# Optimization experiments

Measured on AMD Instinct MI355X. Metric: run time of the kernel, lower is better.

The kernel has to match this reference:

```python
import jax, jax.numpy as jnp
from jax import lax
import numpy as np

H = 64
NS = 20000
NR = 2000
T = 24
ALPHA = 0.5


def _p(key, *shape):
    return jax.random.normal(key, shape, dtype=jnp.float32) * 0.05


def setup_inputs() -> dict:
    key = jax.random.key(0)
    ks = jax.random.split(key, 40)
    inp = {
        "x_store": jax.random.normal(ks[0], (NS, T), dtype=jnp.float32),
        "x_region": jax.random.normal(ks[1], (NR, T), dtype=jnp.float32),
        "edge_ss": jax.random.randint(ks[2], (2, 640000), 0, NS),
        "edge_rs_src": jax.random.randint(ks[3], (160000,), 0, NR),
        "edge_rs_dst": jax.random.randint(ks[4], (160000,), 0, NS),
        "edge_sr_src": jax.random.randint(ks[5], (160000,), 0, NS),
        "edge_sr_dst": jax.random.randint(ks[6], (160000,), 0, NR),
        # LSTM pretransform params (torch gate order i,f,g,o)
        "Wih_s": _p(ks[7], 4 * H, 1), "Whh_s": _p(ks[8], 4 * H, H),
        "bih_s": _p(ks[9], 4 * H), "bhh_s": _p(ks[10], 4 * H),
        "Wih_r": _p(ks[11], 4 * H, 1), "Whh_r": _p(ks[12], 4 * H, H),
        "bih_r": _p(ks[13], 4 * H), "bhh_r": _p(ks[14], 4 * H),
        # DirSageConv (store-store)
        "W_s2d": _p(ks[15], H, H), "b_s2d": _p(ks[16], H),
        "W_d2s": _p(ks[17], H, H), "b_d2s": _p(ks[18], H),
        "W_self": _p(ks[19], H, H), "b_self": _p(ks[20], H),
        # SAGEConv region->store (lin_l w/ bias, lin_r no bias)
        "Wl_rs": _p(ks[21], H, H), "bl_rs": _p(ks[22], H), "Wr_rs": _p(ks[23], H, H),
        # SAGEConv store->region
        "Wl_sr": _p(ks[24], H, H), "bl_sr": _p(ks[25], H), "Wr_sr": _p(ks[26], H, H),
        # final linear
        "Wf": _p(ks[27], H, H), "bf": _p(ks[28], H),
    }
    return inp


def lstm_last(x, Wih, Whh, bih, bhh):
    # x: [N, T] scalar sequences (input_size=1). Returns last hidden state [N, H].
    N = x.shape[0]
    w_in = Wih[:, 0]  # [4H]
    b = bih + bhh

    def step(carry, xt):
        h, c = carry
        gates = xt[:, None] * w_in[None, :] + h @ Whh.T + b  # [N, 4H]
        i, f, g, o = jnp.split(gates, 4, axis=1)
        c = jax.nn.sigmoid(f) * c + jax.nn.sigmoid(i) * jnp.tanh(g)
        h = jax.nn.sigmoid(o) * jnp.tanh(c)
        return (h, c), None

    z = jnp.zeros((N, Whh.shape[1]), x.dtype)
    (h, _), _ = lax.scan(step, (z, z), x.T)
    return h


def mean_aggr(feats, dst_idx, num_dst):
    # mean of gathered edge messages per destination node (0 for isolated nodes)
    s = jax.ops.segment_sum(feats, dst_idx, num_segments=num_dst)
    cnt = jax.ops.segment_sum(jnp.ones(dst_idx.shape, feats.dtype), dst_idx, num_segments=num_dst)
    return s / jnp.maximum(cnt, 1.0)[:, None]


def reference(x_store, x_region, edge_ss, edge_rs_src, edge_rs_dst,
              edge_sr_src, edge_sr_dst,
              Wih_s, Whh_s, bih_s, bhh_s, Wih_r, Whh_r, bih_r, bhh_r,
              W_s2d, b_s2d, W_d2s, b_d2s, W_self, b_self,
              Wl_rs, bl_rs, Wr_rs, Wl_sr, bl_sr, Wr_sr, Wf, bf):
    # per-node-type LSTM pretransform -> [N, H]
    hs = lstm_last(x_store, Wih_s, Whh_s, bih_s, bhh_s)
    hr = lstm_last(x_region, Wih_r, Whh_r, bih_r, bhh_r)

    # DirSageConv on (store, link, store)
    src, dst = edge_ss[0], edge_ss[1]
    a_fwd = mean_aggr(hs[src], dst, NS) @ W_s2d.T + b_s2d   # src -> dst
    a_rev = mean_aggr(hs[dst], src, NS) @ W_d2s.T + b_d2s   # dst -> src
    dir_out = hs @ W_self.T + b_self + (1.0 - ALPHA) * a_fwd + ALPHA * a_rev

    # SAGEConv (region, influences, store)
    rs_out = mean_aggr(hr[edge_rs_src], edge_rs_dst, NS) @ Wl_rs.T + bl_rs + hs @ Wr_rs.T

    # SAGEConv (store, rev_influences, region)
    sr_out = mean_aggr(hs[edge_sr_src], edge_sr_dst, NR) @ Wl_sr.T + bl_sr + hr @ Wr_sr.T

    # HeteroConv aggr='mean' over edge types per dst node type
    store_h = (dir_out + rs_out) * 0.5
    region_h = sr_out

    # residual + relu
    store_h = jax.nn.relu(store_h + hs)
    region_h = jax.nn.relu(region_h + hr)  # computed as in torch, unused by output

    return store_h @ Wf.T + bf
```

## Files before the change

kernel.cpp:

```cpp
#include <hip/hip_runtime.h>
#include <hip/hip_bf16.h>

#define TT 24
#define NSTORE 20000
#define NREGION 2000
#define NE_SS 640000
#define NE_RS 160000
#define BN 32
#define SUBS 96
#define NGRP 8
#define CAPF 80
#define CAPS 32
#define POISON ((int)0xAAAAAAAAu)

typedef __attribute__((ext_vector_type(8))) short bf16x8;
typedef __attribute__((ext_vector_type(4))) float f32x4;
typedef __attribute__((ext_vector_type(4))) int int4v;

__device__ __forceinline__ float rcpf(float x) { return __builtin_amdgcn_rcpf(x); }
__device__ __forceinline__ float sigm(float x) { return rcpf(1.0f + __expf(-x)); }
__device__ __forceinline__ float tanh_(float x) { return fmaf(-2.0f, rcpf(1.0f + __expf(2.0f * x)), 1.0f); }

__device__ __forceinline__ short f2bs(float x) {
    __hip_bfloat16 h = __float2bfloat16(x);
    return *reinterpret_cast<short*>(&h);
}
__device__ __forceinline__ bf16x8 pack8(float4 a, float4 b) {
    bf16x8 r;
    r[0] = f2bs(a.x); r[1] = f2bs(a.y); r[2] = f2bs(a.z); r[3] = f2bs(a.w);
    r[4] = f2bs(b.x); r[5] = f2bs(b.y); r[6] = f2bs(b.z); r[7] = f2bs(b.w);
    return r;
}
__device__ __forceinline__ unsigned packbf2(float lo, float hi) {
    return ((unsigned)(unsigned short)f2bs(hi) << 16) | (unsigned)(unsigned short)f2bs(lo);
}
__device__ __forceinline__ float bf_lo(unsigned u) { return __uint_as_float(u << 16); }
__device__ __forceinline__ float bf_hi(unsigned u) { return __uint_as_float(u & 0xffff0000u); }

__device__ __forceinline__ f32x4 mfma16(bf16x8 a, bf16x8 b, f32x4 c) {
    return __builtin_amdgcn_mfma_f32_16x16x32_bf16(a, b, c, 0, 0, 0);
}

__global__ __launch_bounds__(256)
void fill_seg(const int* __restrict__ ss_src, const int* __restrict__ ss_dst,
              const int* __restrict__ rs_src, const int* __restrict__ rs_dst,
              int* __restrict__ curF, int* __restrict__ curR, int* __restrict__ curS,
              int* __restrict__ eidF, int* __restrict__ eidR, int* __restrict__ eidS)
{
    const int tid = threadIdx.x;
    const int fb = (int)blockIdx.x;
    const int g = fb & (NGRP - 1);
    const int sub = fb / NGRP;
    const int lo = g * (NSTORE / NGRP), hi = lo + NSTORE / NGRP;
    const int stride = SUBS * 256;

    for (int t = sub * 256 + tid; t < NE_SS / 4; t += stride) {
        const int4v s4 = __builtin_nontemporal_load(&((const int4v*)ss_src)[t]);
        const int4v d4 = __builtin_nontemporal_load(&((const int4v*)ss_dst)[t]);
        #pragma unroll
        for (int e = 0; e < 4; ++e) {
            const int se = s4[e], de = d4[e];
            if (de >= lo && de < hi) {
                int p = atomicAdd(&curF[de], 1) - POISON;
                if (p < CAPF) eidF[de * CAPF + p] = se;
            }
            if (se >= lo && se < hi) {
                int p = atomicAdd(&curR[se], 1) - POISON;
                if (p < CAPF) eidR[se * CAPF + p] = de;
            }
        }
    }
    for (int t = sub * 256 + tid; t < NE_RS / 4; t += stride) {
        const int4v s4 = __builtin_nontemporal_load(&((const int4v*)rs_src)[t]);
        const int4v d4 = __builtin_nontemporal_load(&((const int4v*)rs_dst)[t]);
        #pragma unroll
        for (int e = 0; e < 4; ++e) {
            const int se = s4[e], de = d4[e];
            if (de >= lo && de < hi) {
                int p = atomicAdd(&curS[de], 1) - POISON;
                if (p < CAPS) eidS[de * CAPS + p] = se;
            }
        }
    }
}

__global__ __launch_bounds__(256)
void lstm_only(const float* __restrict__ xs, const float* __restrict__ WihS,
               const float* __restrict__ WhhS, const float* __restrict__ bihS,
               const float* __restrict__ bhhS,
               const float* __restrict__ xr, const float* __restrict__ WihR,
               const float* __restrict__ WhhR, const float* __restrict__ bihR,
               const float* __restrict__ bhhR,
               unsigned* __restrict__ hsOut, unsigned* __restrict__ hrOut,
               int nBlocksStore)
{
    const int tid = threadIdx.x;

    __shared__ unsigned hbU[2][32][36];
    __shared__ float xbuf[BN][25];

    const float *x, *Wih, *Whh, *bih, *bhh;
    unsigned* hout; int N, node0;
    if ((int)blockIdx.x < nBlocksStore) {
        x = xs; Wih = WihS; Whh = WhhS; bih = bihS; bhh = bhhS;
        hout = hsOut; N = NSTORE; node0 = blockIdx.x * BN;
    } else {
        x = xr; Wih = WihR; Whh = WhhR; bih = bihR; bhh = bhhR;
        hout = hrOut; N = NREGION; node0 = ((int)blockIdx.x - nBlocksStore) * BN;
    }

    const int w = tid >> 6, lane = tid & 63;
    const int l15 = lane & 15, q = lane >> 4;

    for (int i = tid; i < BN * TT; i += 256) {
        int n = i / TT, t = i - n * TT;
        int gn = node0 + n;
        xbuf[n][t] = (gn < N) ? x[gn * TT + t] : 0.0f;
    }

    bf16x8 Bf[4][2];
    #pragma unroll
    for (int g = 0; g < 4; ++g)
        #pragma unroll
        for (int kt = 0; kt < 2; ++kt) {
            const float* wrow = Whh + (g * 64 + (w << 4) + l15) * 64 + q * 8 + kt * 32;
            float4 v0 = *(const float4*)wrow;
            float4 v1 = *(const float4*)(wrow + 4);
            Bf[g][kt] = pack8(v0, v1);
        }

    float win[4], bsum[4];
    #pragma unroll
    for (int g = 0; g < 4; ++g) {
        int gi = g * 64 + (w << 4) + l15;
        win[g]  = Wih[gi];
        bsum[g] = bih[gi] + bhh[gi];
    }

    __syncthreads();

    float cc[2][4], hv[2][4];
    #pragma unroll
    for (int m = 0; m < 2; ++m)
        #pragma unroll
        for (int r = 0; r < 4; ++r) cc[m][r] = 0.0f;

    for (int t = 0; t < TT; ++t) {
        const int cur = t & 1, prev = cur ^ 1;

        bf16x8 Af[2][2];
        if (t > 0) {
            #pragma unroll
            for (int m = 0; m < 2; ++m)
                #pragma unroll
                for (int kt = 0; kt < 2; ++kt)
                    Af[m][kt] = *(const bf16x8*)&hbU[prev][l15 + 16 * m][(q << 2) + (kt << 4)];
        }

        f32x4 acc[4][2];
        float xv[2][4];
        #pragma unroll
        for (int m = 0; m < 2; ++m)
            #pragma unroll
            for (int r = 0; r < 4; ++r) xv[m][r] = xbuf[16 * m + q * 4 + r][t];
        #pragma unroll
        for (int g = 0; g < 4; ++g)
            #pragma unroll
            for (int m = 0; m < 2; ++m)
                #pragma unroll
                for (int r = 0; r < 4; ++r)
                    acc[g][m][r] = fmaf(xv[m][r], win[g], bsum[g]);

        if (t > 0) {
            #pragma unroll
            for (int g = 0; g < 4; ++g)
                #pragma unroll
                for (int m = 0; m < 2; ++m) {
                    acc[g][m] = mfma16(Af[m][0], Bf[g][0], acc[g][m]);
                    acc[g][m] = mfma16(Af[m][1], Bf[g][1], acc[g][m]);
                }
        }

        #pragma unroll
        for (int m = 0; m < 2; ++m)
            #pragma unroll
            for (int r = 0; r < 4; ++r) {
                float ig = sigm(acc[0][m][r]);
                float fg = sigm(acc[1][m][r]);
                float gg = tanh_(acc[2][m][r]);
                float og = sigm(acc[3][m][r]);
                float cn = fmaf(fg, cc[m][r], ig * gg);
                cc[m][r] = cn;
                hv[m][r] = og * tanh_(cn);
            }

        #pragma unroll
        for (int m = 0; m < 2; ++m)
            #pragma unroll
            for (int r = 0; r < 4; ++r) {
                float other = __shfl_xor(hv[m][r], 1);
                if ((l15 & 1) == 0)
                    hbU[cur][16 * m + 4 * q + r][(w << 3) + (l15 >> 1)] = packbf2(hv[m][r], other);
            }
        __syncthreads();
    }

    for (int i = tid; i < 32 * 32; i += 256) {
        int n = i >> 5, kp = i & 31;
        int gn = node0 + n;
        if (gn < N) hout[gn * 32 + kp] = hbU[1][n][kp];
    }
}

__global__ __launch_bounds__(256)
void gather_means(const unsigned* __restrict__ hsU, const unsigned* __restrict__ hrU,
                  const int* __restrict__ curF, const int* __restrict__ curR,
                  const int* __restrict__ curS,
                  const int* __restrict__ eidF, const int* __restrict__ eidR,
                  const int* __restrict__ eidS,
                  unsigned* __restrict__ xcatU)
{
    const int id = blockIdx.x * 4 + (threadIdx.x >> 6);
    const int lane = threadIdx.x & 63;
    const int sec = id / NSTORE;
    const int n   = id - sec * NSTORE;
    const int o8 = lane >> 3, l7 = lane & 7;

    unsigned* row = xcatU + (size_t)n * 128;

    if (sec == 0 && lane < 32) row[lane] = hsU[n * 32 + lane];

    const unsigned* feat = (sec == 2) ? hrU : hsU;
    const int* seg; int cnt, cap;
    if (sec == 0)      { seg = eidF + n * CAPF; cnt = curF[n] - POISON; cap = CAPF; }
    else if (sec == 1) { seg = eidR + n * CAPF; cnt = curR[n] - POISON; cap = CAPF; }
    else               { seg = eidS + n * CAPS; cnt = curS[n] - POISON; cap = CAPS; }
    int e = cnt < cap ? cnt : cap;

    float a[8];
    #pragma unroll
    for (int k = 0; k < 8; ++k) a[k] = 0.0f;

    for (int i = 0; i < e; i += 16) {
        int i0 = i + o8;
        if (i0 < e) {
            uint4 u = *(const uint4*)&feat[seg[i0] * 32 + 4 * l7];
            a[0] += bf_lo(u.x); a[1] += bf_hi(u.x);
            a[2] += bf_lo(u.y); a[3] += bf_hi(u.y);
            a[4] += bf_lo(u.z); a[5] += bf_hi(u.z);
            a[6] += bf_lo(u.w); a[7] += bf_hi(u.w);
        }
        int i1 = i + 8 + o8;
        if (i1 < e) {
            uint4 u = *(const uint4*)&feat[seg[i1] * 32 + 4 * l7];
            a[0] += bf_lo(u.x); a[1] += bf_hi(u.x);
            a[2] += bf_lo(u.y); a[3] += bf_hi(u.y);
            a[4] += bf_lo(u.z); a[5] += bf_hi(u.z);
            a[6] += bf_lo(u.w); a[7] += bf_hi(u.w);
        }
    }
    #pragma unroll
    for (int k = 0; k < 8; ++k) {
        a[k] += __shfl_xor(a[k], 8);
        a[k] += __shfl_xor(a[k], 16);
        a[k] += __shfl_xor(a[k], 32);
    }
    float c = rcpf(fmaxf((float)cnt, 1.0f));
    if (lane < 8) {
        uint4 o;
        o.x = packbf2(a[0] * c, a[1] * c);
        o.y = packbf2(a[2] * c, a[3] * c);
        o.z = packbf2(a[4] * c, a[5] * c);
        o.w = packbf2(a[6] * c, a[7] * c);
        *(uint4*)&row[(sec + 1) * 32 + 4 * l7] = o;
    }
}

__global__ __launch_bounds__(256, 2)
void combine_mm(const unsigned* __restrict__ xcatU,
                const float* __restrict__ Ws2d, const float* __restrict__ bs2d,
                const float* __restrict__ Wd2s, const float* __restrict__ bd2s,
                const float* __restrict__ Wself, const float* __restrict__ bself,
                const float* __restrict__ Wlrs, const float* __restrict__ blrs,
                const float* __restrict__ Wrrs,
                const float* __restrict__ Wfm, const float* __restrict__ bfv,
                float* __restrict__ out)
{
    __shared__ float Xs[64][68];
    __shared__ float Ps[64][64];
    __shared__ float Us[64][68];
    __shared__ float Wfs[64][68];
    __shared__ float biasc[64];

    const int tid = threadIdx.x;
    const int node0 = blockIdx.x * 64;

    for (int i = tid; i < 4096; i += 256) {
        int jp = i >> 6, j = i & 63;
        Wfs[j][jp] = Wfm[i];
    }
    if (tid < 64)
        biasc[tid] = bself[tid] + 0.5f * bs2d[tid] + 0.5f * bd2s[tid] + blrs[tid];

    const int jg = tid & 15, ng = tid >> 4;
    const int j0 = jg * 4, n0 = ng * 4;

    float acc[4][4];
    #pragma unroll
    for (int dn = 0; dn < 4; ++dn)
        #pragma unroll
        for (int dj = 0; dj < 4; ++dj) acc[dn][dj] = 0.0f;

    const int sj = tid >> 2, skb = tid & 3;

    for (int ci = 0; ci < 4; ++ci) {
        const int c = (ci + 1) & 3;
        __syncthreads();

        {
            int n = tid >> 2;
            int gn = node0 + n; if (gn > NSTORE - 1) gn = NSTORE - 1;
            const unsigned* src = xcatU + (size_t)gn * 128 + c * 32 + (tid & 3) * 8;
            uint4 u0 = *(const uint4*)src;
            uint4 u1 = *(const uint4*)(src + 4);
            unsigned uu[8] = {u0.x, u0.y, u0.z, u0.w, u1.x, u1.y, u1.z, u1.w};
            int k0 = (tid & 3) * 16;
            #pragma unroll
            for (int e = 0; e < 8; ++e) {
                Xs[k0 + 2 * e][n]     = bf_lo(uu[e]);
                Xs[k0 + 2 * e + 1][n] = bf_hi(uu[e]);
            }
        }
        {
            const float* W1; float scale;
            if (c == 0)      { W1 = Wself; scale = 1.0f; }
            else if (c == 1) { W1 = Ws2d;  scale = 0.5f; }
            else if (c == 2) { W1 = Wd2s;  scale = 0.5f; }
            else             { W1 = Wlrs;  scale = 1.0f; }
            #pragma unroll
            for (int qq = 0; qq < 4; ++qq) {
                int k0 = skb * 16 + qq * 4;
                float4 v = *(const float4*)(W1 + sj * 64 + k0);
                if (c == 0) {
                    float4 v2 = *(const float4*)(Wrrs + sj * 64 + k0);
                    v.x += v2.x; v.y += v2.y; v.z += v2.z; v.w += v2.w;
                } else {
                    v.x *= scale; v.y *= scale; v.z *= scale; v.w *= scale;
                }
                Ps[k0][sj] = v.x; Ps[k0 + 1][sj] = v.y;
                Ps[k0 + 2][sj] = v.z; Ps[k0 + 3][sj] = v.w;
            }
        }
        __syncthreads();

        #pragma unroll 4
        for (int k = 0; k < 64; ++k) {
            float4 wv = *(const float4*)&Ps[k][j0];
            float4 xv = *(const float4*)&Xs[k][n0];
            float x4[4] = {xv.x, xv.y, xv.z, xv.w};
            float w4[4] = {wv.x, wv.y, wv.z, wv.w};
            #pragma unroll
            for (int dn = 0; dn < 4; ++dn)
                #pragma unroll
                for (int dj = 0; dj < 4; ++dj)
                    acc[dn][dj] = fmaf(x4[dn], w4[dj], acc[dn][dj]);
        }
    }

    #pragma unroll
    for (int dn = 0; dn < 4; ++dn)
        #pragma unroll
        for (int dj = 0; dj < 4; ++dj) {
            float h = Xs[j0 + dj][n0 + dn];
            float u = fmaxf(fmaf(0.5f, acc[dn][dj] + biasc[j0 + dj], h), 0.0f);
            Us[j0 + dj][n0 + dn] = u;
        }
    __syncthreads();

    float o[4][4];
    #pragma unroll
    for (int dn = 0; dn < 4; ++dn)
        #pragma unroll
        for (int dj = 0; dj < 4; ++dj) o[dn][dj] = 0.0f;

    #pragma unroll 4
    for (int k = 0; k < 64; ++k) {
        float4 wv = *(const float4*)&Wfs[k][j0];
        float4 uv = *(const float4*)&Us[k][n0];
        float u4[4] = {uv.x, uv.y, uv.z, uv.w};
        float w4[4] = {wv.x, wv.y, wv.z, wv.w};
        #pragma unroll
        for (int dn = 0; dn < 4; ++dn)
            #pragma unroll
            for (int dj = 0; dj < 4; ++dj)
                o[dn][dj] = fmaf(u4[dn], w4[dj], o[dn][dj]);
    }

    float4 bfe = *(const float4*)(bfv + j0);
    #pragma unroll
    for (int dn = 0; dn < 4; ++dn) {
        int gn = node0 + n0 + dn;
        if (gn < NSTORE) {
            float4 v = make_float4(o[dn][0] + bfe.x, o[dn][1] + bfe.y,
                                   o[dn][2] + bfe.z, o[dn][3] + bfe.w);
            *(float4*)&out[gn * 64 + j0] = v;
        }
    }
}

extern "C" void kernel_launch(void* const* d_in, const int* in_sizes, int n_in,
                              void* d_out, int out_size, void* d_ws, size_t ws_size,
                              hipStream_t stream)
{
    const float* xs     = (const float*)d_in[0];
    const float* xr     = (const float*)d_in[1];
    const int*   e_ss   = (const int*)d_in[2];
    const int*   rs_src = (const int*)d_in[3];
    const int*   rs_dst = (const int*)d_in[4];
    const float* WihS = (const float*)d_in[7];
    const float* WhhS = (const float*)d_in[8];
    const float* bihS = (const float*)d_in[9];
    const float* bhhS = (const float*)d_in[10];
    const float* WihR = (const float*)d_in[11];
    const float* WhhR = (const float*)d_in[12];
    const float* bihR = (const float*)d_in[13];
    const float* bhhR = (const float*)d_in[14];
    const float* Ws2d = (const float*)d_in[15];
    const float* bs2d = (const float*)d_in[16];
    const float* Wd2s = (const float*)d_in[17];
    const float* bd2s = (const float*)d_in[18];
    const float* Wself = (const float*)d_in[19];
    const float* bself = (const float*)d_in[20];
    const float* Wlrs = (const float*)d_in[21];
    const float* blrs = (const float*)d_in[22];
    const float* Wrrs = (const float*)d_in[23];
    const float* Wfm = (const float*)d_in[27];
    const float* bfv = (const float*)d_in[28];

    const int* ss_src = e_ss;
    const int* ss_dst = e_ss + NE_SS;

    unsigned* hsU   = (unsigned*)d_ws;
    unsigned* hrU   = hsU + 640000;
    unsigned* xcatU = hrU + 64000;
    int*      ib    = (int*)(xcatU + 2560000);
    int* curF = ib;
    int* curR = ib + 20000;
    int* curS = ib + 40000;
    int* eidF = ib + 60000;
    int* eidR = eidF + NSTORE * CAPF;
    int* eidS = eidR + NSTORE * CAPF;

    const int storeBlocks  = (NSTORE + BN - 1) / BN;
    const int regionBlocks = (NREGION + BN - 1) / BN;
    const int lstmBlocks   = storeBlocks + regionBlocks;
    const int fillBlocks   = NGRP * SUBS;

    fill_seg<<<fillBlocks, 256, 0, stream>>>(ss_src, ss_dst, rs_src, rs_dst,
                                             curF, curR, curS, eidF, eidR, eidS);

    lstm_only<<<lstmBlocks, 256, 0, stream>>>(
        xs, WihS, WhhS, bihS, bhhS, xr, WihR, WhhR, bihR, bhhR,
        hsU, hrU, storeBlocks);

    gather_means<<<3 * NSTORE / 4, 256, 0, stream>>>(hsU, hrU,
                                                     curF, curR, curS,
                                                     eidF, eidR, eidS, xcatU);

    combine_mm<<<(NSTORE + 63) / 64, 256, 0, stream>>>(xcatU,
                                                       Ws2d, bs2d, Wd2s, bd2s,
                                                       Wself, bself, Wlrs, blrs, Wrrs,
                                                       Wfm, bfv, (float*)d_out);
}
```

Baseline: 312.7 us.

## Fuse edge-bucketing fill into LSTM kernel and split LSTM work across 8 waves

The separate fill_seg launch is merged into the LSTM kernel as extra blocks, so edge bucketing with atomics runs concurrently with the latency-bound recurrent LSTM blocks instead of before them. The LSTM block grows to 512 threads, with each wave handling one 16-node half of the tile instead of both. This halves per-wave serial MFMA and activation work per timestep and raises wave-level parallelism. The cost is more threads per block and fewer fill blocks, which may lower occupancy or lengthen the fill tail.

```diff
diff --git a/kernel.cpp b/kernel.cpp
--- a/kernel.cpp
+++ b/kernel.cpp
@@ -7,7 +7,7 @@
 #define NE_SS 640000
 #define NE_RS 160000
 #define BN 32
-#define SUBS 96
+#define SUBS 48
 #define NGRP 8
 #define CAPF 80
 #define CAPS 32
@@ -41,60 +41,59 @@
     return __builtin_amdgcn_mfma_f32_16x16x32_bf16(a, b, c, 0, 0, 0);
 }
 
-__global__ __launch_bounds__(256)
-void fill_seg(const int* __restrict__ ss_src, const int* __restrict__ ss_dst,
-              const int* __restrict__ rs_src, const int* __restrict__ rs_dst,
-              int* __restrict__ curF, int* __restrict__ curR, int* __restrict__ curS,
-              int* __restrict__ eidF, int* __restrict__ eidR, int* __restrict__ eidS)
-{
-    const int tid = threadIdx.x;
-    const int fb = (int)blockIdx.x;
-    const int g = fb & (NGRP - 1);
-    const int sub = fb / NGRP;
-    const int lo = g * (NSTORE / NGRP), hi = lo + NSTORE / NGRP;
-    const int stride = SUBS * 256;
-
-    for (int t = sub * 256 + tid; t < NE_SS / 4; t += stride) {
-        const int4v s4 = __builtin_nontemporal_load(&((const int4v*)ss_src)[t]);
-        const int4v d4 = __builtin_nontemporal_load(&((const int4v*)ss_dst)[t]);
-        #pragma unroll
-        for (int e = 0; e < 4; ++e) {
-            const int se = s4[e], de = d4[e];
-            if (de >= lo && de < hi) {
-                int p = atomicAdd(&curF[de], 1) - POISON;
-                if (p < CAPF) eidF[de * CAPF + p] = se;
-            }
-            if (se >= lo && se < hi) {
-                int p = atomicAdd(&curR[se], 1) - POISON;
-                if (p < CAPF) eidR[se * CAPF + p] = de;
-            }
-        }
-    }
-    for (int t = sub * 256 + tid; t < NE_RS / 4; t += stride) {
-        const int4v s4 = __builtin_nontemporal_load(&((const int4v*)rs_src)[t]);
-        const int4v d4 = __builtin_nontemporal_load(&((const int4v*)rs_dst)[t]);
-        #pragma unroll
-        for (int e = 0; e < 4; ++e) {
-            const int se = s4[e], de = d4[e];
-            if (de >= lo && de < hi) {
-                int p = atomicAdd(&curS[de], 1) - POISON;
-                if (p < CAPS) eidS[de * CAPS + p] = se;
-            }
-        }
-    }
-}
-
-__global__ __launch_bounds__(256)
-void lstm_only(const float* __restrict__ xs, const float* __restrict__ WihS,
+__global__ __launch_bounds__(512)
+void lstm_fill(const float* __restrict__ xs, const float* __restrict__ WihS,
                const float* __restrict__ WhhS, const float* __restrict__ bihS,
                const float* __restrict__ bhhS,
                const float* __restrict__ xr, const float* __restrict__ WihR,
                const float* __restrict__ WhhR, const float* __restrict__ bihR,
                const float* __restrict__ bhhR,
                unsigned* __restrict__ hsOut, unsigned* __restrict__ hrOut,
-               int nBlocksStore)
+               const int* __restrict__ ss_src, const int* __restrict__ ss_dst,
+               const int* __restrict__ rs_src, const int* __restrict__ rs_dst,
+               int* __restrict__ curF, int* __restrict__ curR, int* __restrict__ curS,
+               int* __restrict__ eidF, int* __restrict__ eidR, int* __restrict__ eidS,
+               int nBlocksStore, int nBlocksLstm)
 {
     const int tid = threadIdx.x;
+
+    if ((int)blockIdx.x >= nBlocksLstm) {
+        const int fb = (int)blockIdx.x - nBlocksLstm;
+        const int g = fb & (NGRP - 1);
+        const int sub = fb >> 3;
+        const int lo = g * (NSTORE / NGRP), hi = lo + NSTORE / NGRP;
+        const int stride = SUBS * 512;
+
+        for (int t = sub * 512 + tid; t < NE_SS / 4; t += stride) {
+            const int4v s4 = __builtin_nontemporal_load(&((const int4v*)ss_src)[t]);
+            const int4v d4 = __builtin_nontemporal_load(&((const int4v*)ss_dst)[t]);
+            #pragma unroll
+            for (int e = 0; e < 4; ++e) {
+                const int se = s4[e], de = d4[e];
+                if (de >= lo && de < hi) {
+                    int p = atomicAdd(&curF[de], 1) - POISON;
+                    if (p < CAPF) eidF[de * CAPF + p] = se;
+                }
+                if (se >= lo && se < hi) {
+                    int p = atomicAdd(&curR[se], 1) - POISON;
+                    if (p < CAPF) eidR[se * CAPF + p] = de;
+                }
+            }
+        }
+        for (int t = sub * 512 + tid; t < NE_RS / 4; t += stride) {
+            const int4v s4 = __builtin_nontemporal_load(&((const int4v*)rs_src)[t]);
+            const int4v d4 = __builtin_nontemporal_load(&((const int4v*)rs_dst)[t]);
+            #pragma unroll
+            for (int e = 0; e < 4; ++e) {
+                const int se = s4[e], de = d4[e];
+                if (de >= lo && de < hi) {
+                    int p = atomicAdd(&curS[de], 1) - POISON;
+                    if (p < CAPS) eidS[de * CAPS + p] = se;
+                }
+            }
+        }
+        return;
+    }
 
     __shared__ unsigned hbU[2][32][36];
     __shared__ float xbuf[BN][25];
@@ -109,10 +108,13 @@
         hout = hrOut; N = NREGION; node0 = ((int)blockIdx.x - nBlocksStore) * BN;
     }
 
-    const int w = tid >> 6, lane = tid & 63;
+    const int w8 = tid >> 6;
+    const int wg = w8 & 3;
+    const int mm = w8 >> 2;
+    const int lane = tid & 63;
     const int l15 = lane & 15, q = lane >> 4;
 
-    for (int i = tid; i < BN * TT; i += 256) {
+    for (int i = tid; i < BN * TT; i += 512) {
         int n = i / TT, t = i - n * TT;
         int gn = node0 + n;
         xbuf[n][t] = (gn < N) ? x[gn * TT + t] : 0.0f;
@@ -123,7 +125,7 @@
     for (int g = 0; g < 4; ++g)
         #pragma unroll
         for (int kt = 0; kt < 2; ++kt) {
-            const float* wrow = Whh + (g * 64 + (w << 4) + l15) * 64 + q * 8 + kt * 32;
+            const float* wrow = Whh + (g * 64 + (wg << 4) + l15) * 64 + q * 8 + kt * 32;
             float4 v0 = *(const float4*)wrow;
             float4 v1 = *(const float4*)(wrow + 4);
             Bf[g][kt] = pack8(v0, v1);
@@ -132,80 +134,66 @@
     float win[4], bsum[4];
     #pragma unroll
     for (int g = 0; g < 4; ++g) {
-        int gi = g * 64 + (w << 4) + l15;
+        int gi = g * 64 + (wg << 4) + l15;
         win[g]  = Wih[gi];
         bsum[g] = bih[gi] + bhh[gi];
     }
 
     __syncthreads();
 
-    float cc[2][4], hv[2][4];
-    #pragma unroll
-    for (int m = 0; m < 2; ++m)
-        #pragma unroll
-        for (int r = 0; r < 4; ++r) cc[m][r] = 0.0f;
+    float cc[4], hv[4];
+    #pragma unroll
+    for (int r = 0; r < 4; ++r) cc[r] = 0.0f;
 
     for (int t = 0; t < TT; ++t) {
         const int cur = t & 1, prev = cur ^ 1;
 
-        bf16x8 Af[2][2];
+        bf16x8 Af[2];
         if (t > 0) {
             #pragma unroll
-            for (int m = 0; m < 2; ++m)
-                #pragma unroll
-                for (int kt = 0; kt < 2; ++kt)
-                    Af[m][kt] = *(const bf16x8*)&hbU[prev][l15 + 16 * m][(q << 2) + (kt << 4)];
-        }
-
-        f32x4 acc[4][2];
-        float xv[2][4];
-        #pragma unroll
-        for (int m = 0; m < 2; ++m)
-            #pragma unroll
-            for (int r = 0; r < 4; ++r) xv[m][r] = xbuf[16 * m + q * 4 + r][t];
+            for (int kt = 0; kt < 2; ++kt)
+                Af[kt] = *(const bf16x8*)&hbU[prev][l15 + 16 * mm][(q << 2) + (kt << 4)];
+        }
+
+        f32x4 acc[4];
+        float xv[4];
+        #pragma unroll
+        for (int r = 0; r < 4; ++r) xv[r] = xbuf[16 * mm + q * 4 + r][t];
         #pragma unroll
         for (int g = 0; g < 4; ++g)
             #pragma unroll
-            for (int m = 0; m < 2; ++m)
-                #pragma unroll
-                for (int r = 0; r < 4; ++r)
-                    acc[g][m][r] = fmaf(xv[m][r], win[g], bsum[g]);
+            for (int r = 0; r < 4; ++r)
+                acc[g][r] = fmaf(xv[r], win[g], bsum[g]);
 
         if (t > 0) {
             #pragma unroll
-            for (int g = 0; g < 4; ++g)
-                #pragma unroll
-                for (int m = 0; m < 2; ++m) {
-                    acc[g][m] = mfma16(Af[m][0], Bf[g][0], acc[g][m]);
-                    acc[g][m] = mfma16(Af[m][1], Bf[g][1], acc[g][m]);
-                }
-        }
-
-        #pragma unroll
-        for (int m = 0; m < 2; ++m)
-            #pragma unroll
-            for (int r = 0; r < 4; ++r) {
-                float ig = sigm(acc[0][m][r]);
-                float fg = sigm(acc[1][m][r]);
-                float gg = tanh_(acc[2][m][r]);
-                float og = sigm(acc[3][m][r]);
-                float cn = fmaf(fg, cc[m][r], ig * gg);
-                cc[m][r] = cn;
-                hv[m][r] = og * tanh_(cn);
+            for (int g = 0; g < 4; ++g) {
+                acc[g] = mfma16(Af[0], Bf[g][0], acc[g]);
+                acc[g] = mfma16(Af[1], Bf[g][1], acc[g]);
             }
-
-        #pragma unroll
-        for (int m = 0; m < 2; ++m)
-            #pragma unroll
-            for (int r = 0; r < 4; ++r) {
-                float other = __shfl_xor(hv[m][r], 1);
-                if ((l15 & 1) == 0)
-                    hbU[cur][16 * m + 4 * q + r][(w << 3) + (l15 >> 1)] = packbf2(hv[m][r], other);
-            }
+        }
+
+        #pragma unroll
+        for (int r = 0; r < 4; ++r) {
+            float ig = sigm(acc[0][r]);
+            float fg = sigm(acc[1][r]);
+            float gg = tanh_(acc[2][r]);
+            float og = sigm(acc[3][r]);
+            float cn = fmaf(fg, cc[r], ig * gg);
+            cc[r] = cn;
+            hv[r] = og * tanh_(cn);
+        }
+
+        #pragma unroll
+        for (int r = 0; r < 4; ++r) {
+            float other = __shfl_xor(hv[r], 1);
+            if ((l15 & 1) == 0)
+                hbU[cur][16 * mm + 4 * q + r][(wg << 3) + (l15 >> 1)] = packbf2(hv[r], other);
+        }
         __syncthreads();
     }
 
-    for (int i = tid; i < 32 * 32; i += 256) {
+    for (int i = tid; i < 32 * 32; i += 512) {
         int n = i >> 5, kp = i & 31;
         int gn = node0 + n;
         if (gn < N) hout[gn * 32 + kp] = hbU[1][n][kp];
@@ -456,12 +444,11 @@
     const int lstmBlocks   = storeBlocks + regionBlocks;
     const int fillBlocks   = NGRP * SUBS;
 
-    fill_seg<<<fillBlocks, 256, 0, stream>>>(ss_src, ss_dst, rs_src, rs_dst,
-                                             curF, curR, curS, eidF, eidR, eidS);
-
-    lstm_only<<<lstmBlocks, 256, 0, stream>>>(
+    lstm_fill<<<lstmBlocks + fillBlocks, 512, 0, stream>>>(
         xs, WihS, WhhS, bihS, bhhS, xr, WihR, WhhR, bihR, bhhR,
-        hsU, hrU, storeBlocks);
+        hsU, hrU, ss_src, ss_dst, rs_src, rs_dst,
+        curF, curR, curS, eidF, eidR, eidS,
+        storeBlocks, lstmBlocks);
 
     gather_means<<<3 * NSTORE / 4, 256, 0, stream>>>(hsU, hrU,
                                                      curF, curR, curS,
```

After: 281.6 us. -9.9%, faster.

## Make each LSTM wave own 16 nodes and all gates, removing block barriers

Applied to the files above, without the earlier changes.

The LSTM recurrence is reorganized so each wavefront processes 16 nodes across all 256 gate columns, holding the full Whh in bf16 MFMA fragments in registers. The per-timestep block-wide __syncthreads used to exchange hidden state between waves goes away, and the hidden-state exchange now goes through a per-wave XOR-swizzled LDS buffer meant to avoid bank conflicts. Blocks cover 64 nodes instead of 32. In exchange each wave holds many more registers (32 bf16x8 fragments plus 16-wide bias and input weights), which may reduce occupancy or cause spills. Correctness within a wave relies on lockstep LDS ordering with no explicit wave barrier between the hidden-state writes and the next step's reads.

```diff
diff --git a/kernel.cpp b/kernel.cpp
--- a/kernel.cpp
+++ b/kernel.cpp
@@ -6,7 +6,6 @@
 #define NREGION 2000
 #define NE_SS 640000
 #define NE_RS 160000
-#define BN 32
 #define SUBS 96
 #define NGRP 8
 #define CAPF 80
@@ -85,7 +84,7 @@
 }
 
 __global__ __launch_bounds__(256)
-void lstm_only(const float* __restrict__ xs, const float* __restrict__ WihS,
+void lstm_wave(const float* __restrict__ xs, const float* __restrict__ WihS,
                const float* __restrict__ WhhS, const float* __restrict__ bihS,
                const float* __restrict__ bhhS,
                const float* __restrict__ xr, const float* __restrict__ WihR,
@@ -94,121 +93,118 @@
                unsigned* __restrict__ hsOut, unsigned* __restrict__ hrOut,
                int nBlocksStore)
 {
+    __shared__ float xbuf[64][25];
+    __shared__ unsigned hls[4][512];
+
     const int tid = threadIdx.x;
-
-    __shared__ unsigned hbU[2][32][36];
-    __shared__ float xbuf[BN][25];
 
     const float *x, *Wih, *Whh, *bih, *bhh;
     unsigned* hout; int N, node0;
     if ((int)blockIdx.x < nBlocksStore) {
         x = xs; Wih = WihS; Whh = WhhS; bih = bihS; bhh = bhhS;
-        hout = hsOut; N = NSTORE; node0 = blockIdx.x * BN;
+        hout = hsOut; N = NSTORE; node0 = blockIdx.x * 64;
     } else {
         x = xr; Wih = WihR; Whh = WhhR; bih = bihR; bhh = bhhR;
-        hout = hrOut; N = NREGION; node0 = ((int)blockIdx.x - nBlocksStore) * BN;
-    }
-
-    const int w = tid >> 6, lane = tid & 63;
-    const int l15 = lane & 15, q = lane >> 4;
-
-    for (int i = tid; i < BN * TT; i += 256) {
+        hout = hrOut; N = NREGION; node0 = ((int)blockIdx.x - nBlocksStore) * 64;
+    }
+
+    for (int i = tid; i < 64 * TT; i += 256) {
         int n = i / TT, t = i - n * TT;
         int gn = node0 + n;
         xbuf[n][t] = (gn < N) ? x[gn * TT + t] : 0.0f;
     }
-
-    bf16x8 Bf[4][2];
-    #pragma unroll
-    for (int g = 0; g < 4; ++g)
+    __syncthreads();
+
+    const int w = tid >> 6, lane = tid & 63;
+    const int l15 = lane & 15, q = lane >> 4;
+    const int wnode0 = node0 + w * 16;
+    if (wnode0 >= N) return;
+
+    bf16x8 Bf[16][2];
+    #pragma unroll
+    for (int nt = 0; nt < 16; ++nt)
         #pragma unroll
         for (int kt = 0; kt < 2; ++kt) {
-            const float* wrow = Whh + (g * 64 + (w << 4) + l15) * 64 + q * 8 + kt * 32;
+            const float* wrow = Whh + (nt * 16 + l15) * 64 + q * 8 + kt * 32;
             float4 v0 = *(const float4*)wrow;
             float4 v1 = *(const float4*)(wrow + 4);
-            Bf[g][kt] = pack8(v0, v1);
-        }
-
-    float win[4], bsum[4];
-    #pragma unroll
-    for (int g = 0; g < 4; ++g) {
-        int gi = g * 64 + (w << 4) + l15;
-        win[g]  = Wih[gi];
-        bsum[g] = bih[gi] + bhh[gi];
-    }
-
-    __syncthreads();
-
-    float cc[2][4], hv[2][4];
-    #pragma unroll
-    for (int m = 0; m < 2; ++m)
-        #pragma unroll
-        for (int r = 0; r < 4; ++r) cc[m][r] = 0.0f;
+            Bf[nt][kt] = pack8(v0, v1);
+        }
+
+    float win[16], bsum[16];
+    #pragma unroll
+    for (int nt = 0; nt < 16; ++nt) {
+        int gi = nt * 16 + l15;
+        win[nt]  = Wih[gi];
+        bsum[nt] = bih[gi] + bhh[gi];
+    }
+
+    float cc[4][4];
+    #pragma unroll
+    for (int cn = 0; cn < 4; ++cn)
+        #pragma unroll
+        for (int r = 0; r < 4; ++r) cc[cn][r] = 0.0f;
+
+    const int nodeC = q * 4;
 
     for (int t = 0; t < TT; ++t) {
-        const int cur = t & 1, prev = cur ^ 1;
-
-        bf16x8 Af[2][2];
+        bf16x8 af0, af1;
         if (t > 0) {
-            #pragma unroll
-            for (int m = 0; m < 2; ++m)
-                #pragma unroll
-                for (int kt = 0; kt < 2; ++kt)
-                    Af[m][kt] = *(const bf16x8*)&hbU[prev][l15 + 16 * m][(q << 2) + (kt << 4)];
-        }
-
-        f32x4 acc[4][2];
-        float xv[2][4];
-        #pragma unroll
-        for (int m = 0; m < 2; ++m)
-            #pragma unroll
-            for (int r = 0; r < 4; ++r) xv[m][r] = xbuf[16 * m + q * 4 + r][t];
-        #pragma unroll
-        for (int g = 0; g < 4; ++g)
-            #pragma unroll
-            for (int m = 0; m < 2; ++m)
+            unsigned wa0 = (unsigned)((l15 * 32 + q * 4) ^ ((l15 & 7) << 2));
+            unsigned wa1 = (unsigned)((l15 * 32 + q * 4 + 16) ^ ((l15 & 7) << 2));
+            af0 = *(const bf16x8*)&hls[w][wa0];
+            af1 = *(const bf16x8*)&hls[w][wa1];
+        }
+
+        float xv[4];
+        #pragma unroll
+        for (int r = 0; r < 4; ++r) xv[r] = xbuf[w * 16 + nodeC + r][t];
+
+        float hv[4][4];
+        #pragma unroll
+        for (int cn = 0; cn < 4; ++cn) {
+            f32x4 acc[4];
+            #pragma unroll
+            for (int gt = 0; gt < 4; ++gt) {
+                const int nt = cn + 4 * gt;
                 #pragma unroll
                 for (int r = 0; r < 4; ++r)
-                    acc[g][m][r] = fmaf(xv[m][r], win[g], bsum[g]);
-
-        if (t > 0) {
-            #pragma unroll
-            for (int g = 0; g < 4; ++g)
-                #pragma unroll
-                for (int m = 0; m < 2; ++m) {
-                    acc[g][m] = mfma16(Af[m][0], Bf[g][0], acc[g][m]);
-                    acc[g][m] = mfma16(Af[m][1], Bf[g][1], acc[g][m]);
+                    acc[gt][r] = fmaf(xv[r], win[nt], bsum[nt]);
+                if (t > 0) {
+                    acc[gt] = mfma16(af0, Bf[nt][0], acc[gt]);
+                    acc[gt] = mfma16(af1, Bf[nt][1], acc[gt]);
                 }
-        }
-
-        #pragma unroll
-        for (int m = 0; m < 2; ++m)
+            }
             #pragma unroll
             for (int r = 0; r < 4; ++r) {
-                float ig = sigm(acc[0][m][r]);
-                float fg = sigm(acc[1][m][r]);
-                float gg = tanh_(acc[2][m][r]);
-                float og = sigm(acc[3][m][r]);
-                float cn = fmaf(fg, cc[m][r], ig * gg);
-                cc[m][r] = cn;
-                hv[m][r] = og * tanh_(cn);
-            }
-
-        #pragma unroll
-        for (int m = 0; m < 2; ++m)
+                float ig = sigm(acc[0][r]);
+                float fg = sigm(acc[1][r]);
+                float gg = tanh_(acc[2][r]);
+                float og = sigm(acc[3][r]);
+                float cnew = fmaf(fg, cc[cn][r], ig * gg);
+                cc[cn][r] = cnew;
+                hv[cn][r] = og * tanh_(cnew);
+            }
+        }
+
+        #pragma unroll
+        for (int cn = 0; cn < 4; ++cn)
             #pragma unroll
             for (int r = 0; r < 4; ++r) {
-                float other = __shfl_xor(hv[m][r], 1);
-                if ((l15 & 1) == 0)
-                    hbU[cur][16 * m + 4 * q + r][(w << 3) + (l15 >> 1)] = packbf2(hv[m][r], other);
-            }
-        __syncthreads();
-    }
-
-    for (int i = tid; i < 32 * 32; i += 256) {
-        int n = i >> 5, kp = i & 31;
-        int gn = node0 + n;
-        if (gn < N) hout[gn * 32 + kp] = hbU[1][n][kp];
+                float other = __shfl_xor(hv[cn][r], 1);
+                if ((l15 & 1) == 0) {
+                    int node = nodeC + r;
+                    unsigned wi = (unsigned)((node * 32 + cn * 8 + (l15 >> 1))
+                                             ^ ((node & 7) << 2));
+                    hls[w][wi] = packbf2(hv[cn][r], other);
+                }
+            }
+    }
+
+    for (int i = lane; i < 512; i += 64) {
+        int node = i >> 5, kp = i & 31;
+        unsigned wi = (unsigned)((node * 32 + kp) ^ ((node & 7) << 2));
+        hout[(wnode0 + node) * 32 + kp] = hls[w][wi];
     }
 }
 
@@ -451,17 +447,16 @@
     int* eidR = eidF + NSTORE * CAPF;
     int* eidS = eidR + NSTORE * CAPF;
 
-    const int storeBlocks  = (NSTORE + BN - 1) / BN;
-    const int regionBlocks = (NREGION + BN - 1) / BN;
-    const int lstmBlocks   = storeBlocks + regionBlocks;
-    const int fillBlocks   = NGRP * SUBS;
+    const int fillBlocks    = NGRP * SUBS;
+    const int storeBlocksW  = (NSTORE + 63) / 64;
+    const int regionBlocksW = (NREGION + 63) / 64;
 
     fill_seg<<<fillBlocks, 256, 0, stream>>>(ss_src, ss_dst, rs_src, rs_dst,
                                              curF, curR, curS, eidF, eidR, eidS);
 
-    lstm_only<<<lstmBlocks, 256, 0, stream>>>(
+    lstm_wave<<<storeBlocksW + regionBlocksW, 256, 0, stream>>>(
         xs, WihS, WhhS, bihS, bhhS, xr, WihR, WhhR, bihR, bhhR,
-        hsU, hrU, storeBlocks);
+        hsU, hrU, storeBlocksW);
 
     gather_means<<<3 * NSTORE / 4, 256, 0, stream>>>(hsU, hrU,
                                                      curF, curR, curS,
```

After: 384.8 us. 1.23x slower.
